# Optimization experiments

Hardware: AMD Instinct MI355X
Metric: run time of the kernel (lower is better)

Reference implementation:

```python
import jax, jax.numpy as jnp
import numpy as np

N, IN_DIM, OUT_DIM, H = 1024, 128, 128, 4
D = OUT_DIM // H  # head_dim = 32
NEG_SLOPE = 0.2
MASK_VAL = -1e9
LN_EPS = 1e-5


def setup_inputs() -> dict:
    key = jax.random.key(0)
    k = jax.random.split(key, 8)
    h = jax.random.normal(k[0], (N, IN_DIM), dtype=jnp.float32)
    adj = jax.random.randint(k[1], (N, N), 0, 2, dtype=jnp.int32)
    adj = adj.at[jnp.arange(N), jnp.arange(N)].set(1)  # self-loops
    s = 1.0 / np.sqrt(IN_DIM)
    W_l = jax.random.normal(k[2], (IN_DIM, OUT_DIM), dtype=jnp.float32) * s
    W_r = jax.random.normal(k[3], (IN_DIM, OUT_DIM), dtype=jnp.float32) * s
    W_v = jax.random.normal(k[4], (IN_DIM, OUT_DIM), dtype=jnp.float32) * s
    a = jax.random.normal(k[5], (D,), dtype=jnp.float32) * (1.0 / np.sqrt(D))
    ln_g = jnp.ones((OUT_DIM,), dtype=jnp.float32)
    ln_b = jnp.zeros((OUT_DIM,), dtype=jnp.float32)
    return {"h": h, "adj": adj, "W_l": W_l, "W_r": W_r, "W_v": W_v,
            "a": a, "ln_g": ln_g, "ln_b": ln_b}


def reference(h, adj, W_l, W_r, W_v, a, ln_g, ln_b):
    n = h.shape[0]
    Wlh = (h @ W_l).reshape(n, H, D)   # [N,H,D]
    Wrh = (h @ W_r).reshape(n, H, D)   # [N,H,D]
    # pairwise additive scores: pair[i,j,h,d] = Wlh[i] + Wrh[j]
    pair = Wlh[:, None, :, :] + Wrh[None, :, :, :]          # [N,N,H,D]
    pair = jnp.where(pair >= 0, pair, NEG_SLOPE * pair)      # leaky_relu(0.2)
    e = jnp.einsum('ijhd,d->ijh', pair, a)                   # [N,N,H]
    mask = (adj != 0)[:, :, None]                            # [N,N,1]
    e = jnp.where(mask, e, MASK_VAL)
    alpha = jax.nn.softmax(e, axis=1)                        # softmax over j
    v = (h @ W_v).reshape(n, H, D)                           # [N,H,D]
    agg = jnp.einsum('ijh,jhd->ihd', alpha, v).reshape(n, OUT_DIM)
    mu = jnp.mean(agg, axis=-1, keepdims=True)
    var = jnp.mean((agg - mu) ** 2, axis=-1, keepdims=True)
    y = (agg - mu) * jax.lax.rsqrt(var + LN_EPS) * ln_g + ln_b
    return jax.nn.relu(y)
```

## Files before the change

### kernel.cpp

```cpp
#include <hip/hip_runtime.h>
#include <cstdint>

typedef _Float16 f16;
typedef _Float16 f16x2 __attribute__((ext_vector_type(2)));
typedef _Float16 f16x4 __attribute__((ext_vector_type(4)));
typedef _Float16 f16x8 __attribute__((ext_vector_type(8)));
typedef float    f32x4 __attribute__((ext_vector_type(4)));
typedef unsigned short u16;
typedef unsigned int   u32;
typedef unsigned long long u64;

#define LOG2E 1.44269504088896340736f

__device__ __forceinline__ f16x2 habs2(f16x2 v) {
    union { f16x2 h; u32 u; } x; x.h = v; x.u &= 0x7FFF7FFFu; return x.h;
}
#if __has_builtin(__builtin_amdgcn_fdot2)
__device__ __forceinline__ float fdot2f(f16x2 a, f16x2 b, float c) {
    return __builtin_amdgcn_fdot2(a, b, c, false);
}
#else
__device__ __forceinline__ float fdot2f(f16x2 a, f16x2 b, float c) {
    return c + (float)a.x * (float)b.x + (float)a.y * (float)b.y;
}
#endif
#if __has_builtin(__builtin_amdgcn_exp2f)
#define EXP2F __builtin_amdgcn_exp2f
#else
#define EXP2F exp2f
#endif

__global__ __launch_bounds__(384) void k1_proj(
        const float* __restrict__ Wl, const float* __restrict__ Wr,
        const float* __restrict__ Wv, const float* __restrict__ h,
        const float* __restrict__ a_,
        f16* __restrict__ Wlh, f16* __restrict__ WrL, f16* __restrict__ VL,
        float* __restrict__ AL, float* __restrict__ BR) {
    __shared__ __align__(16) f16 hS[4][128];
    const int t    = threadIdx.x;
    const int i0   = blockIdx.x * 4;
    const int wsel = t >> 7, col = t & 127;
    const int lane = t & 63;

    for (int e = t; e < 512; e += 384)
        ((f16*)hS)[e] = (f16)h[i0 * 128 + e];

    const float* W = (wsel == 0) ? Wl : ((wsel == 1) ? Wr : Wv);
    f16x2 w2[64];
    #pragma unroll
    for (int c2 = 0; c2 < 64; c2++) {
        f16x2 v;
        v.x = (f16)W[(2 * c2) * 128 + col];
        v.y = (f16)W[(2 * c2 + 1) * 128 + col];
        w2[c2] = v;
    }
    const float asc = 0.6f * a_[col & 31];
    __syncthreads();

    #pragma unroll
    for (int i = 0; i < 4; i++) {
        const int j = i0 + i;
        const f16x2* hr = (const f16x2*)hS[i];
        float acc = 0.f;
        #pragma unroll
        for (int c2 = 0; c2 < 64; c2++) acc = fdot2f(hr[c2], w2[c2], acc);
        const f16 hv = (f16)acc;
        const int hh = col >> 5, dd = col & 31;
        if (wsel == 0) {
            Wlh[j * 128 + col] = hv;
        } else if (wsel == 1) {
            WrL[((hh * 8 + (dd >> 2)) * 1024 + j) * 4 + (dd & 3)] = hv;
        } else {
            VL[(hh * 32 + dd) * 1024 + j] = hv;
        }
        if (wsel < 2) {
            float part = asc * acc;
            #pragma unroll
            for (int off = 1; off < 32; off <<= 1) part += __shfl_xor(part, off);
            if ((lane & 31) == 0) {
                if (wsel == 0) AL[j * 4 + hh] = part;
                else           BR[hh * 1024 + j] = part;
            }
        }
    }
}

__global__ __launch_bounds__(512) void GATv2Layer_84447646974220_kernel(
        const f16* __restrict__ Wlh, const f16* __restrict__ WrL,
        const f16* __restrict__ VL,  const int* __restrict__ adj,
        const float* __restrict__ AL, const float* __restrict__ BR,
        const float* __restrict__ a_, const float* __restrict__ ln_g,
        const float* __restrict__ ln_b, float* __restrict__ out) {

    __shared__ __align__(16) f16 ep[4][4][1024];
    __shared__ float aggS[2][4][128];
    __shared__ float redM[2][4][4];
    __shared__ float redS[2][4][4];
    __shared__ u64 amaskS[4][16];

    const int t    = threadIdx.x;
    const int w    = t >> 6;
    const int lane = t & 63;
    const int hh   = w & 3;
    const int half = w >> 2;
    const int i0   = blockIdx.x * 4;

    {
        const int r  = w & 3;
        const int w0 = (w >> 2) * 8;
        #pragma unroll
        for (int c = 0; c < 8; c++) {
            int av = adj[(i0 + r) * 1024 + (w0 + c) * 64 + lane];
            u64 m = __ballot(av != 0);
            if (lane == 0) amaskS[r][w0 + c] = m;
        }
    }

    f16x2 q2[16];
    #pragma unroll
    for (int d2 = 0; d2 < 16; d2++) {
        f16x2 q; q.x = (f16)(0.4f * a_[2 * d2]); q.y = (f16)(0.4f * a_[2 * d2 + 1]);
        q2[d2] = q;
    }
    f16x2 wl2[4][16];
    float al[4];
    #pragma unroll
    for (int ii = 0; ii < 4; ii++) {
        const f16x2* src = (const f16x2*)(Wlh + (i0 + ii) * 128 + hh * 32);
        #pragma unroll
        for (int c2 = 0; c2 < 16; c2++) wl2[ii][c2] = src[c2];
        al[ii] = AL[(i0 + ii) * 4 + hh];
    }
    __syncthreads();

    float maxE[4];
    #pragma unroll
    for (int ii = 0; ii < 4; ii++) maxE[ii] = -__builtin_inff();

    auto LD = [&](int jb, f16x4 (&wr)[8], float &bj) {
        int j = half * 512 + jb * 64 + lane;
        #pragma unroll
        for (int c = 0; c < 8; c++)
            wr[c] = *(const f16x4*)(WrL + ((hh * 8 + c) * 1024 + j) * 4);
        bj = BR[hh * 1024 + j];
    };
    auto CMP = [&](int jb, const f16x4 (&wr)[8], float bj) {
        int j = half * 512 + jb * 64 + lane;
        float e[4];
        #pragma unroll
        for (int ii = 0; ii < 4; ii++) e[ii] = al[ii];
        #pragma unroll
        for (int c = 0; c < 8; c++) {
            #pragma unroll
            for (int ii = 0; ii < 4; ii++) {
                f16x2 t0 = wl2[ii][2 * c]     + wr[c].lo;
                f16x2 t1 = wl2[ii][2 * c + 1] + wr[c].hi;
                e[ii] = fdot2f(q2[2 * c],     habs2(t0), e[ii]);
                e[ii] = fdot2f(q2[2 * c + 1], habs2(t1), e[ii]);
            }
        }
        #pragma unroll
        for (int ii = 0; ii < 4; ii++) {
            bool ok = (amaskS[ii][half * 8 + jb] >> lane) & 1ull;
            float v = ok ? (e[ii] + bj) : -__builtin_inff();
            maxE[ii] = fmaxf(maxE[ii], v);
            ep[hh][ii][j] = (f16)v;
        }
    };

    f16x4 wrA[8], wrB[8];
    float bjA, bjB;

    LD(0, wrA, bjA);
    #pragma unroll 1
    for (int jb = 0; jb < 8; jb += 2) {
        LD(jb + 1, wrB, bjB);
        CMP(jb, wrA, bjA);
        if (jb + 2 < 8) LD(jb + 2, wrA, bjA);
        CMP(jb + 1, wrB, bjB);
    }

    #pragma unroll
    for (int ii = 0; ii < 4; ii++) {
        float M = maxE[ii];
        #pragma unroll
        for (int off = 32; off > 0; off >>= 1) M = fmaxf(M, __shfl_xor(M, off));
        maxE[ii] = M;
    }
    #pragma unroll
    for (int ii = 0; ii < 4; ii++) {
        float Mk = fmaxf(maxE[ii], -3.0e38f);
        f16x8 v0 = *(f16x8*)&ep[hh][ii][half * 512 + lane * 8];
        float pb[8], l = 0.f;
        #pragma unroll
        for (int e = 0; e < 8; e++) pb[e] = EXP2F(((float)v0[e] - Mk) * LOG2E);
        #pragma unroll
        for (int e = 0; e < 8; e++) { v0[e] = (f16)pb[e]; l += pb[e]; }
        *(f16x8*)&ep[hh][ii][half * 512 + lane * 8] = v0;
        #pragma unroll
        for (int off = 32; off > 0; off >>= 1) l += __shfl_xor(l, off);
        if (lane == 0) { redM[half][hh][ii] = maxE[ii]; redS[half][hh][ii] = l; }
    }
    __syncthreads();

    float lr[4];
    #pragma unroll
    for (int ii = 0; ii < 4; ii++) {
        float M0 = redM[0][hh][ii], M1 = redM[1][hh][ii];
        float M  = fmaxf(M0, M1);
        float s0 = EXP2F((M0 - M) * LOG2E);
        float s1 = EXP2F((M1 - M) * LOG2E);
        float l  = redS[0][hh][ii] * s0 + redS[1][hh][ii] * s1;
        lr[ii] = (half == 0 ? s0 : s1) / l;
    }

    f32x4 acc0 = {0.f, 0.f, 0.f, 0.f}, acc1 = {0.f, 0.f, 0.f, 0.f};
    const int q8  = (lane >> 4) << 3;
    const int m3  = lane & 3;
    const int n15 = lane & 15;

    #pragma unroll 2
    for (int jt4 = 0; jt4 < 4; jt4++) {
        int jt = half * 4 + jt4;
        #pragma unroll
        for (int kk = 0; kk < 4; kk++) {
            int ko = jt * 128 + kk * 32 + q8;
            f16x8 af = *(const f16x8*)&ep[hh][m3][ko];
            f16x8 b0 = *(const f16x8*)(VL + (hh * 32 + n15) * 1024 + ko);
            f16x8 b1 = *(const f16x8*)(VL + (hh * 32 + 16 + n15) * 1024 + ko);
            acc0 = __builtin_amdgcn_mfma_f32_16x16x32_f16(af, b0, acc0, 0, 0, 0);
            acc1 = __builtin_amdgcn_mfma_f32_16x16x32_f16(af, b1, acc1, 0, 0, 0);
        }
    }

    if (lane < 16) {
        #pragma unroll
        for (int r = 0; r < 4; r++) {
            aggS[half][r][hh * 32 + lane]      = acc0[r] * lr[r];
            aggS[half][r][hh * 32 + 16 + lane] = acc1[r] * lr[r];
        }
    }
    __syncthreads();

    if (w < 4) {
        float x0 = aggS[0][w][lane]      + aggS[1][w][lane];
        float x1 = aggS[0][w][lane + 64] + aggS[1][w][lane + 64];
        float s = x0 + x1, sq = x0 * x0 + x1 * x1;
        #pragma unroll
        for (int off = 32; off > 0; off >>= 1) {
            s  += __shfl_xor(s, off);
            sq += __shfl_xor(sq, off);
        }
        float mean = s * (1.f / 128.f);
        float var  = sq * (1.f / 128.f) - mean * mean;
        float rs   = rsqrtf(var + 1e-5f);
        float y0 = fmaxf((x0 - mean) * rs * ln_g[lane]      + ln_b[lane],      0.f);
        float y1 = fmaxf((x1 - mean) * rs * ln_g[lane + 64] + ln_b[lane + 64], 0.f);
        out[(i0 + w) * 128 + lane]      = y0;
        out[(i0 + w) * 128 + 64 + lane] = y1;
    }
}

extern "C" void kernel_launch(void* const* d_in, const int* in_sizes, int n_in,
                              void* d_out, int out_size, void* d_ws, size_t ws_size,
                              hipStream_t stream) {
    const float* h   = (const float*)d_in[0];
    const int*   adj = (const int*)d_in[1];
    const float* Wl  = (const float*)d_in[2];
    const float* Wr  = (const float*)d_in[3];
    const float* Wv  = (const float*)d_in[4];
    const float* a_  = (const float*)d_in[5];
    const float* g_  = (const float*)d_in[6];
    const float* b_  = (const float*)d_in[7];
    float* out = (float*)d_out;

    char* ws = (char*)d_ws;
    f16*   Wlh = (f16*)(ws);
    f16*   WrL = (f16*)(ws + 262144);
    f16*   VL  = (f16*)(ws + 524288);
    float* AL  = (float*)(ws + 786432);
    float* BR  = (float*)(ws + 802816);

    k1_proj<<<256, 384, 0, stream>>>(Wl, Wr, Wv, h, a_, Wlh, WrL, VL, AL, BR);
    GATv2Layer_84447646974220_kernel<<<256, 512, 0, stream>>>(
        Wlh, WrL, VL, adj, AL, BR, a_, g_, b_, out);
}
```

Measured before the change: 97.95 us.

## Split neighbor range across four wave groups with 1024-thread blocks

Doubles the block size to 1024 threads so each head's 1024 neighbors are split into four quarters instead of two halves, with the softmax max/sum and aggregation partials merged across four groups in shared memory. The aim is more waves in flight per block and a shorter serial loop per wave over only 256 neighbors. The hand-written software prefetch (double-buffered loads) is dropped in favour of a plain loop unrolled by two. The larger block raises register pressure per CU under launch_bounds(1024), which may force spills or lower occupancy, and adds reduction work.

```diff
diff --git a/kernel.cpp b/kernel.cpp
--- a/kernel.cpp
+++ b/kernel.cpp
@@ -85,7 +85,7 @@
     }
 }
 
-__global__ __launch_bounds__(512) void GATv2Layer_84447646974220_kernel(
+__global__ __launch_bounds__(1024) void GATv2Layer_84447646974220_kernel(
         const f16* __restrict__ Wlh, const f16* __restrict__ WrL,
         const f16* __restrict__ VL,  const int* __restrict__ adj,
         const float* __restrict__ AL, const float* __restrict__ BR,
@@ -93,23 +93,23 @@
         const float* __restrict__ ln_b, float* __restrict__ out) {
 
     __shared__ __align__(16) f16 ep[4][4][1024];
-    __shared__ float aggS[2][4][128];
-    __shared__ float redM[2][4][4];
-    __shared__ float redS[2][4][4];
+    __shared__ float aggS[4][4][128];
+    __shared__ float redM[4][4][4];
+    __shared__ float redS[4][4][4];
     __shared__ u64 amaskS[4][16];
 
     const int t    = threadIdx.x;
     const int w    = t >> 6;
     const int lane = t & 63;
     const int hh   = w & 3;
-    const int half = w >> 2;
+    const int q    = w >> 2;
     const int i0   = blockIdx.x * 4;
 
     {
         const int r  = w & 3;
-        const int w0 = (w >> 2) * 8;
-        #pragma unroll
-        for (int c = 0; c < 8; c++) {
+        const int w0 = q * 4;
+        #pragma unroll
+        for (int c = 0; c < 4; c++) {
             int av = adj[(i0 + r) * 1024 + (w0 + c) * 64 + lane];
             u64 m = __ballot(av != 0);
             if (lane == 0) amaskS[r][w0 + c] = m;
@@ -119,8 +119,8 @@
     f16x2 q2[16];
     #pragma unroll
     for (int d2 = 0; d2 < 16; d2++) {
-        f16x2 q; q.x = (f16)(0.4f * a_[2 * d2]); q.y = (f16)(0.4f * a_[2 * d2 + 1]);
-        q2[d2] = q;
+        f16x2 qq; qq.x = (f16)(0.4f * a_[2 * d2]); qq.y = (f16)(0.4f * a_[2 * d2 + 1]);
+        q2[d2] = qq;
     }
     f16x2 wl2[4][16];
     float al[4];
@@ -137,15 +137,15 @@
     #pragma unroll
     for (int ii = 0; ii < 4; ii++) maxE[ii] = -__builtin_inff();
 
-    auto LD = [&](int jb, f16x4 (&wr)[8], float &bj) {
-        int j = half * 512 + jb * 64 + lane;
+    #pragma unroll 2
+    for (int jb = 0; jb < 4; jb++) {
+        const int j = q * 256 + jb * 64 + lane;
+        f16x4 wr[8];
         #pragma unroll
         for (int c = 0; c < 8; c++)
             wr[c] = *(const f16x4*)(WrL + ((hh * 8 + c) * 1024 + j) * 4);
-        bj = BR[hh * 1024 + j];
-    };
-    auto CMP = [&](int jb, const f16x4 (&wr)[8], float bj) {
-        int j = half * 512 + jb * 64 + lane;
+        const float bj = BR[hh * 1024 + j];
+
         float e[4];
         #pragma unroll
         for (int ii = 0; ii < 4; ii++) e[ii] = al[ii];
@@ -161,23 +161,11 @@
         }
         #pragma unroll
         for (int ii = 0; ii < 4; ii++) {
-            bool ok = (amaskS[ii][half * 8 + jb] >> lane) & 1ull;
+            bool ok = (amaskS[ii][q * 4 + jb] >> lane) & 1ull;
             float v = ok ? (e[ii] + bj) : -__builtin_inff();
             maxE[ii] = fmaxf(maxE[ii], v);
             ep[hh][ii][j] = (f16)v;
         }
-    };
-
-    f16x4 wrA[8], wrB[8];
-    float bjA, bjB;
-
-    LD(0, wrA, bjA);
-    #pragma unroll 1
-    for (int jb = 0; jb < 8; jb += 2) {
-        LD(jb + 1, wrB, bjB);
-        CMP(jb, wrA, bjA);
-        if (jb + 2 < 8) LD(jb + 2, wrA, bjA);
-        CMP(jb + 1, wrB, bjB);
     }
 
     #pragma unroll
@@ -190,16 +178,16 @@
     #pragma unroll
     for (int ii = 0; ii < 4; ii++) {
         float Mk = fmaxf(maxE[ii], -3.0e38f);
-        f16x8 v0 = *(f16x8*)&ep[hh][ii][half * 512 + lane * 8];
-        float pb[8], l = 0.f;
-        #pragma unroll
-        for (int e = 0; e < 8; e++) pb[e] = EXP2F(((float)v0[e] - Mk) * LOG2E);
-        #pragma unroll
-        for (int e = 0; e < 8; e++) { v0[e] = (f16)pb[e]; l += pb[e]; }
-        *(f16x8*)&ep[hh][ii][half * 512 + lane * 8] = v0;
+        f16x4 v0 = *(f16x4*)&ep[hh][ii][q * 256 + lane * 4];
+        float pb[4], l = 0.f;
+        #pragma unroll
+        for (int e = 0; e < 4; e++) pb[e] = EXP2F(((float)v0[e] - Mk) * LOG2E);
+        #pragma unroll
+        for (int e = 0; e < 4; e++) { v0[e] = (f16)pb[e]; l += pb[e]; }
+        *(f16x4*)&ep[hh][ii][q * 256 + lane * 4] = v0;
         #pragma unroll
         for (int off = 32; off > 0; off >>= 1) l += __shfl_xor(l, off);
-        if (lane == 0) { redM[half][hh][ii] = maxE[ii]; redS[half][hh][ii] = l; }
+        if (lane == 0) { redM[q][hh][ii] = maxE[ii]; redS[q][hh][ii] = l; }
     }
     __syncthreads();
 
@@ -207,11 +195,16 @@
     #pragma unroll
     for (int ii = 0; ii < 4; ii++) {
         float M0 = redM[0][hh][ii], M1 = redM[1][hh][ii];
-        float M  = fmaxf(M0, M1);
+        float M2 = redM[2][hh][ii], M3 = redM[3][hh][ii];
+        float M  = fmaxf(fmaxf(M0, M1), fmaxf(M2, M3));
         float s0 = EXP2F((M0 - M) * LOG2E);
         float s1 = EXP2F((M1 - M) * LOG2E);
-        float l  = redS[0][hh][ii] * s0 + redS[1][hh][ii] * s1;
-        lr[ii] = (half == 0 ? s0 : s1) / l;
+        float s2 = EXP2F((M2 - M) * LOG2E);
+        float s3 = EXP2F((M3 - M) * LOG2E);
+        float l  = redS[0][hh][ii] * s0 + redS[1][hh][ii] * s1
+                 + redS[2][hh][ii] * s2 + redS[3][hh][ii] * s3;
+        float sq = (q == 0) ? s0 : ((q == 1) ? s1 : ((q == 2) ? s2 : s3));
+        lr[ii] = sq / l;
     }
 
     f32x4 acc0 = {0.f, 0.f, 0.f, 0.f}, acc1 = {0.f, 0.f, 0.f, 0.f};
@@ -219,9 +212,9 @@
     const int m3  = lane & 3;
     const int n15 = lane & 15;
 
-    #pragma unroll 2
-    for (int jt4 = 0; jt4 < 4; jt4++) {
-        int jt = half * 4 + jt4;
+    #pragma unroll
+    for (int jt2 = 0; jt2 < 2; jt2++) {
+        int jt = q * 2 + jt2;
         #pragma unroll
         for (int kk = 0; kk < 4; kk++) {
             int ko = jt * 128 + kk * 32 + q8;
@@ -236,15 +229,17 @@
     if (lane < 16) {
         #pragma unroll
         for (int r = 0; r < 4; r++) {
-            aggS[half][r][hh * 32 + lane]      = acc0[r] * lr[r];
-            aggS[half][r][hh * 32 + 16 + lane] = acc1[r] * lr[r];
+            aggS[q][r][hh * 32 + lane]      = acc0[r] * lr[r];
+            aggS[q][r][hh * 32 + 16 + lane] = acc1[r] * lr[r];
         }
     }
     __syncthreads();
 
     if (w < 4) {
-        float x0 = aggS[0][w][lane]      + aggS[1][w][lane];
-        float x1 = aggS[0][w][lane + 64] + aggS[1][w][lane + 64];
+        float x0 = aggS[0][w][lane]      + aggS[1][w][lane]
+                 + aggS[2][w][lane]      + aggS[3][w][lane];
+        float x1 = aggS[0][w][lane + 64] + aggS[1][w][lane + 64]
+                 + aggS[2][w][lane + 64] + aggS[3][w][lane + 64];
         float s = x0 + x1, sq = x0 * x0 + x1 * x1;
         #pragma unroll
         for (int off = 32; off > 0; off >>= 1) {
@@ -282,6 +277,6 @@
     float* BR  = (float*)(ws + 802816);
 
     k1_proj<<<256, 384, 0, stream>>>(Wl, Wr, Wv, h, a_, Wlh, WrL, VL, AL, BR);
-    GATv2Layer_84447646974220_kernel<<<256, 512, 0, stream>>>(
+    GATv2Layer_84447646974220_kernel<<<256, 1024, 0, stream>>>(
         Wlh, WrL, VL, adj, AL, BR, a_, g_, b_, out);
 }
```

New measurement: 100.3 us. +2.4%, slower.
